# Kernel optimization log

Hardware: AMD Instinct MI355X
Metric: run time of the kernel (lower is better)

Reference implementation:

```python
import jax, jax.numpy as jnp
import numpy as np

PAD_IDX = 0
VOCAB = 60
HIDDEN = 128
BATCH = 1024
SEQ = 256


def setup_inputs() -> dict:
    key = jax.random.key(0)
    ks = jax.random.split(key, 6)
    x = jax.random.randint(ks[0], (BATCH, SEQ), 0, VOCAB, dtype=jnp.int64 if jax.config.jax_enable_x64 else jnp.int32)
    lengths = jax.random.randint(ks[1], (BATCH,), 1, SEQ + 1, dtype=x.dtype)
    emb = jax.random.normal(ks[2], (VOCAB, HIDDEN), dtype=jnp.float32) * 0.1
    emb = emb.at[PAD_IDX].set(0.0)  # nn.Embedding padding_idx row is zero
    W_ih = jax.random.normal(ks[3], (HIDDEN, HIDDEN), dtype=jnp.float32) * (1.0 / np.sqrt(HIDDEN))
    W_hh = jax.random.normal(ks[4], (HIDDEN, HIDDEN), dtype=jnp.float32) * (1.0 / np.sqrt(HIDDEN))
    W_fc = jax.random.normal(ks[5], (VOCAB, HIDDEN), dtype=jnp.float32) * (1.0 / np.sqrt(HIDDEN))
    b_fc = jnp.zeros((VOCAB,), dtype=jnp.float32)
    return {"x": x, "lengths": lengths, "emb": emb, "W_ih": W_ih,
            "W_hh": W_hh, "W_fc": W_fc, "b_fc": b_fc}


def reference(x, lengths, emb, W_ih, W_hh, W_fc, b_fc):
    embedded = emb[x]                      # [B, T, H]
    B = embedded.shape[0]
    h0 = jnp.zeros((B, HIDDEN), dtype=embedded.dtype)

    def step(h_prev, x_t):
        # z_t = x_t @ W_ih^T + h_prev @ W_hh^T ; h_t = tanh(z_t)
        h_t = jnp.tanh(x_t @ W_ih.T + h_prev @ W_hh.T)
        return h_t, h_t

    _, hs = jax.lax.scan(step, h0, jnp.swapaxes(embedded, 0, 1))  # hs: [T, B, H]
    outputs = jnp.swapaxes(hs, 0, 1)       # [B, T, H]
    last_out = jnp.take_along_axis(outputs, (lengths - 1)[:, None, None], axis=1)[:, 0, :]  # [B, H]
    return last_out @ W_fc.T + b_fc[None, :]
```

## Files before the change

### kernel.cpp

```cpp
#include <hip/hip_runtime.h>
#include <hip/hip_bf16.h>

#define BATCH 1024
#define SEQ 256
#define HIDDEN 128
#define VOCAB 60
#define MTILE 16
#define ASTRIDE 136
#define XSTRIDE (SEQ + 1)

typedef _Float16 f16x8 __attribute__((ext_vector_type(8)));
typedef _Float16 f16x4 __attribute__((ext_vector_type(4)));
typedef float f32x4 __attribute__((ext_vector_type(4)));

__device__ __forceinline__ float fast_tanh(float x) {
    float e = __builtin_amdgcn_exp2f(x * 2.8853900817779268f);
    return __builtin_fmaf(-2.0f, __builtin_amdgcn_rcpf(e + 1.0f), 1.0f);
}

__global__ void rnn_prep_embw(const float* __restrict__ emb,
                              const float* __restrict__ W_ih,
                              float* __restrict__ embW) {
    const int v = blockIdx.x;
    const int i = threadIdx.x;
    __shared__ __align__(16) float e[HIDDEN];
    e[i] = emb[v * HIDDEN + i];
    __syncthreads();
    const float4* wrow = (const float4*)(W_ih + i * HIDDEN);
    const float4* e4 = (const float4*)e;
    float a0 = 0.f, a1 = 0.f, a2 = 0.f, a3 = 0.f;
#pragma unroll
    for (int j = 0; j < HIDDEN / 4; ++j) {
        float4 w = wrow[j];
        float4 h = e4[j];
        a0 += w.x * h.x; a1 += w.y * h.y; a2 += w.z * h.z; a3 += w.w * h.w;
    }
    embW[v * HIDDEN + i] = (a0 + a1) + (a2 + a3);
}

__global__ void __launch_bounds__(256)
rnn_mfma(const int* __restrict__ x, const int* __restrict__ lengths,
         const float* __restrict__ embW, const float* __restrict__ W_hh,
         const float* __restrict__ W_fc, const float* __restrict__ b_fc,
         float* __restrict__ out) {
    const int tid = threadIdx.x;
    const int wave = tid >> 6;
    const int lane = tid & 63;
    const int q = lane >> 4;
    const int r16 = lane & 15;
    const int c0 = wave * 32;
    const int b0 = blockIdx.x * MTILE;

    __shared__ __align__(16) _Float16 Ah[2][MTILE][ASTRIDE];
    __shared__ int xs[MTILE][XSTRIDE];
    __shared__ __align__(16) float hfin[MTILE][HIDDEN];
    __shared__ int lenbuf[MTILE];

    for (int idx = tid; idx < MTILE * SEQ; idx += 256) {
        int r = idx >> 8, t = idx & (SEQ - 1);
        xs[r][t] = x[(b0 + r) * SEQ + t];
    }
    if (tid < MTILE) lenbuf[tid] = lengths[b0 + tid];

    for (int idx = tid; idx < 2 * MTILE * ASTRIDE; idx += 256)
        ((_Float16*)Ah)[idx] = (_Float16)0.0f;

    f16x8 Wf[2][4];
#pragma unroll
    for (int nt = 0; nt < 2; ++nt) {
        const float* wrow = W_hh + (c0 + 16 * nt + r16) * HIDDEN + q * 8;
#pragma unroll
        for (int kc = 0; kc < 4; ++kc) {
            const float* p = wrow + kc * 32;
#pragma unroll
            for (int j = 0; j < 8; ++j) Wf[nt][kc][j] = (_Float16)p[j];
        }
    }

    __syncthreads();

    const int mylen = lenbuf[r16];
    int lenmax = 0;
    for (int r = 0; r < MTILE; ++r) lenmax = max(lenmax, lenbuf[r]);

    {
    }
    int tok0 = xs[r16][0];
    const float* eb0 = embW + tok0 * HIDDEN + c0 + 4 * q;
    f32x4 pre0 = *(const f32x4*)eb0;
    f32x4 pre1 = *(const f32x4*)(eb0 + 16);
    int tokn = xs[r16][1 < lenmax ? 1 : 0];

    int cur = 0;
    f32x4 hout0 = {0.f, 0.f, 0.f, 0.f}, hout1 = {0.f, 0.f, 0.f, 0.f};

    for (int t = 0; t < lenmax; ++t) {
        const _Float16* arow = &Ah[cur][r16][q * 8];
        f16x8 H0 = *(const f16x8*)(arow + 0);
        f16x8 H1 = *(const f16x8*)(arow + 32);
        f16x8 H2 = *(const f16x8*)(arow + 64);
        f16x8 H3 = *(const f16x8*)(arow + 96);

        const float* eb = embW + tokn * HIDDEN + c0 + 4 * q;
        f32x4 pn0 = *(const f32x4*)eb;
        f32x4 pn1 = *(const f32x4*)(eb + 16);
        const int t2 = (t + 2 < lenmax) ? t + 2 : lenmax - 1;
        tokn = xs[r16][t2];

        f32x4 a0 = pre0, a1 = pre1;
        f32x4 d0 = {0.f, 0.f, 0.f, 0.f}, d1 = {0.f, 0.f, 0.f, 0.f};
        a0 = __builtin_amdgcn_mfma_f32_16x16x32_f16(Wf[0][0], H0, a0, 0, 0, 0);
        a1 = __builtin_amdgcn_mfma_f32_16x16x32_f16(Wf[1][0], H0, a1, 0, 0, 0);
        d0 = __builtin_amdgcn_mfma_f32_16x16x32_f16(Wf[0][2], H2, d0, 0, 0, 0);
        d1 = __builtin_amdgcn_mfma_f32_16x16x32_f16(Wf[1][2], H2, d1, 0, 0, 0);
        a0 = __builtin_amdgcn_mfma_f32_16x16x32_f16(Wf[0][1], H1, a0, 0, 0, 0);
        a1 = __builtin_amdgcn_mfma_f32_16x16x32_f16(Wf[1][1], H1, a1, 0, 0, 0);
        d0 = __builtin_amdgcn_mfma_f32_16x16x32_f16(Wf[0][3], H3, d0, 0, 0, 0);
        d1 = __builtin_amdgcn_mfma_f32_16x16x32_f16(Wf[1][3], H3, d1, 0, 0, 0);
        f32x4 z0 = a0 + d0;
        f32x4 z1 = a1 + d1;

        f32x4 th0, th1;
#pragma unroll
        for (int v = 0; v < 4; ++v) {
            th0[v] = fast_tanh(z0[v]);
            th1[v] = fast_tanh(z1[v]);
        }
        if (t + 1 == mylen) { hout0 = th0; hout1 = th1; }

        const int nxt = cur ^ 1;
        f16x4 w0, w1;
#pragma unroll
        for (int v = 0; v < 4; ++v) {
            w0[v] = (_Float16)th0[v];
            w1[v] = (_Float16)th1[v];
        }
        *(f16x4*)&Ah[nxt][r16][c0 + 4 * q] = w0;
        *(f16x4*)&Ah[nxt][r16][c0 + 16 + 4 * q] = w1;
        __syncthreads();
        cur = nxt;
        pre0 = pn0; pre1 = pn1;
    }

#pragma unroll
    for (int v = 0; v < 4; ++v) {
        hfin[r16][c0 + 4 * q + v] = hout0[v];
        hfin[r16][c0 + 16 + 4 * q + v] = hout1[v];
    }
    __syncthreads();

    const int r = tid >> 4;
    const int vbase = tid & 15;
    const float4* hv = (const float4*)hfin[r];
    for (int vo = vbase; vo < VOCAB; vo += 16) {
        const float4* wf = (const float4*)(W_fc + vo * HIDDEN);
        float a0 = 0.f, a1 = 0.f, a2 = 0.f, a3 = 0.f;
#pragma unroll
        for (int j = 0; j < HIDDEN / 4; ++j) {
            float4 a = hv[j];
            float4 w = wf[j];
            a0 += a.x * w.x; a1 += a.y * w.y; a2 += a.z * w.z; a3 += a.w * w.w;
        }
        out[(b0 + r) * VOCAB + vo] = (a0 + a1) + (a2 + a3) + b_fc[vo];
    }
}

extern "C" void kernel_launch(void* const* d_in, const int* in_sizes, int n_in,
                              void* d_out, int out_size, void* d_ws, size_t ws_size,
                              hipStream_t stream) {
    const int* x = (const int*)d_in[0];
    const int* lengths = (const int*)d_in[1];
    const float* emb = (const float*)d_in[2];
    const float* W_ih = (const float*)d_in[3];
    const float* W_hh = (const float*)d_in[4];
    const float* W_fc = (const float*)d_in[5];
    const float* b_fc = (const float*)d_in[6];
    float* out = (float*)d_out;

    float* embW = (float*)d_ws;

    rnn_prep_embw<<<VOCAB, HIDDEN, 0, stream>>>(emb, W_ih, embW);
    rnn_mfma<<<BATCH / MTILE, 256, 0, stream>>>(x, lengths, embW, W_hh, W_fc, b_fc, out);
}
```

Baseline: 193.5 us.

## Pack four 16-row batch tiles per 1024-thread block, read tokens from global

Each block now handles 64 batch rows with 16 waves (four 16-row groups sharing the same W_hh column split), so the grid shrinks from 64 to 16 blocks. Token indices are read directly from global memory instead of being staged into shared memory. The tanh outputs are packed to f16 with cvt_pkrtz, and the final hidden state is kept in f16 for the FC layer. Only 16 blocks on a many-CU GPU leaves most CUs idle. Each block's loop also runs to the longest sequence among 64 rows, and one block-wide barrier now syncs 16 waves per step, so this risks a slower recurrence.

```diff
diff --git a/kernel.cpp b/kernel.cpp
--- a/kernel.cpp
+++ b/kernel.cpp
@@ -5,12 +5,13 @@
 #define SEQ 256
 #define HIDDEN 128
 #define VOCAB 60
-#define MTILE 16
+#define NT 4
+#define MROWS (NT * 16)
 #define ASTRIDE 136
-#define XSTRIDE (SEQ + 1)
 
 typedef _Float16 f16x8 __attribute__((ext_vector_type(8)));
 typedef _Float16 f16x4 __attribute__((ext_vector_type(4)));
+typedef _Float16 f16x2 __attribute__((ext_vector_type(2)));
 typedef float f32x4 __attribute__((ext_vector_type(4)));
 
 __device__ __forceinline__ float fast_tanh(float x) {
@@ -38,32 +39,30 @@
     embW[v * HIDDEN + i] = (a0 + a1) + (a2 + a3);
 }
 
-__global__ void __launch_bounds__(256)
+__global__ void __launch_bounds__(1024)
 rnn_mfma(const int* __restrict__ x, const int* __restrict__ lengths,
          const float* __restrict__ embW, const float* __restrict__ W_hh,
          const float* __restrict__ W_fc, const float* __restrict__ b_fc,
          float* __restrict__ out) {
     const int tid = threadIdx.x;
     const int wave = tid >> 6;
+    const int tt = wave >> 2;
+    const int wq = wave & 3;
     const int lane = tid & 63;
     const int q = lane >> 4;
     const int r16 = lane & 15;
-    const int c0 = wave * 32;
-    const int b0 = blockIdx.x * MTILE;
+    const int c0 = wq * 32;
+    const int b0 = blockIdx.x * MROWS;
+    const int rloc = tt * 16 + r16;
+    const int row = b0 + rloc;
 
-    __shared__ __align__(16) _Float16 Ah[2][MTILE][ASTRIDE];
-    __shared__ int xs[MTILE][XSTRIDE];
-    __shared__ __align__(16) float hfin[MTILE][HIDDEN];
-    __shared__ int lenbuf[MTILE];
+    __shared__ __align__(16) _Float16 Ah[2][NT][16][ASTRIDE];
+    __shared__ __align__(16) _Float16 hfin[MROWS][HIDDEN];
+    __shared__ int lenbuf[MROWS];
 
-    for (int idx = tid; idx < MTILE * SEQ; idx += 256) {
-        int r = idx >> 8, t = idx & (SEQ - 1);
-        xs[r][t] = x[(b0 + r) * SEQ + t];
-    }
-    if (tid < MTILE) lenbuf[tid] = lengths[b0 + tid];
-
-    for (int idx = tid; idx < 2 * MTILE * ASTRIDE; idx += 256)
-        ((_Float16*)Ah)[idx] = (_Float16)0.0f;
+    if (tid < MROWS) lenbuf[tid] = lengths[b0 + tid];
+    for (int idx = tid; idx < (int)(sizeof(Ah) / 4); idx += 1024)
+        ((int*)Ah)[idx] = 0;
 
     f16x8 Wf[2][4];
 #pragma unroll
@@ -79,23 +78,22 @@
 
     __syncthreads();
 
-    const int mylen = lenbuf[r16];
     int lenmax = 0;
-    for (int r = 0; r < MTILE; ++r) lenmax = max(lenmax, lenbuf[r]);
+    for (int r = 0; r < MROWS; ++r) lenmax = max(lenmax, lenbuf[r]);
+    const int mylen = lenbuf[rloc];
 
-    {
-    }
-    int tok0 = xs[r16][0];
+    const int* xrow = x + row * SEQ;
+    int tok0 = xrow[0];
     const float* eb0 = embW + tok0 * HIDDEN + c0 + 4 * q;
     f32x4 pre0 = *(const f32x4*)eb0;
     f32x4 pre1 = *(const f32x4*)(eb0 + 16);
-    int tokn = xs[r16][1 < lenmax ? 1 : 0];
+    int tokn = xrow[lenmax > 1 ? 1 : 0];
 
+    uint2 hA = {0u, 0u}, hB = {0u, 0u};
     int cur = 0;
-    f32x4 hout0 = {0.f, 0.f, 0.f, 0.f}, hout1 = {0.f, 0.f, 0.f, 0.f};
 
     for (int t = 0; t < lenmax; ++t) {
-        const _Float16* arow = &Ah[cur][r16][q * 8];
+        const _Float16* arow = &Ah[cur][tt][r16][q * 8];
         f16x8 H0 = *(const f16x8*)(arow + 0);
         f16x8 H1 = *(const f16x8*)(arow + 32);
         f16x8 H2 = *(const f16x8*)(arow + 64);
@@ -105,7 +103,7 @@
         f32x4 pn0 = *(const f32x4*)eb;
         f32x4 pn1 = *(const f32x4*)(eb + 16);
         const int t2 = (t + 2 < lenmax) ? t + 2 : lenmax - 1;
-        tokn = xs[r16][t2];
+        const int tok2 = xrow[t2];
 
         f32x4 a0 = pre0, a1 = pre1;
         f32x4 d0 = {0.f, 0.f, 0.f, 0.f}, d1 = {0.f, 0.f, 0.f, 0.f};
@@ -120,46 +118,43 @@
         f32x4 z0 = a0 + d0;
         f32x4 z1 = a1 + d1;
 
-        f32x4 th0, th1;
-#pragma unroll
-        for (int v = 0; v < 4; ++v) {
-            th0[v] = fast_tanh(z0[v]);
-            th1[v] = fast_tanh(z1[v]);
-        }
-        if (t + 1 == mylen) { hout0 = th0; hout1 = th1; }
+        float t00 = fast_tanh(z0[0]), t01 = fast_tanh(z0[1]);
+        float t02 = fast_tanh(z0[2]), t03 = fast_tanh(z0[3]);
+        float t10 = fast_tanh(z1[0]), t11 = fast_tanh(z1[1]);
+        float t12 = fast_tanh(z1[2]), t13 = fast_tanh(z1[3]);
+
+        uint2 pk0, pk1;
+        pk0.x = __builtin_bit_cast(unsigned int, __builtin_amdgcn_cvt_pkrtz(t00, t01));
+        pk0.y = __builtin_bit_cast(unsigned int, __builtin_amdgcn_cvt_pkrtz(t02, t03));
+        pk1.x = __builtin_bit_cast(unsigned int, __builtin_amdgcn_cvt_pkrtz(t10, t11));
+        pk1.y = __builtin_bit_cast(unsigned int, __builtin_amdgcn_cvt_pkrtz(t12, t13));
+
+        if (t + 1 == mylen) { hA = pk0; hB = pk1; }
 
         const int nxt = cur ^ 1;
-        f16x4 w0, w1;
-#pragma unroll
-        for (int v = 0; v < 4; ++v) {
-            w0[v] = (_Float16)th0[v];
-            w1[v] = (_Float16)th1[v];
-        }
-        *(f16x4*)&Ah[nxt][r16][c0 + 4 * q] = w0;
-        *(f16x4*)&Ah[nxt][r16][c0 + 16 + 4 * q] = w1;
+        *(uint2*)&Ah[nxt][tt][r16][c0 + 4 * q] = pk0;
+        *(uint2*)&Ah[nxt][tt][r16][c0 + 16 + 4 * q] = pk1;
         __syncthreads();
         cur = nxt;
-        pre0 = pn0; pre1 = pn1;
+        pre0 = pn0; pre1 = pn1; tokn = tok2;
     }
 
-#pragma unroll
-    for (int v = 0; v < 4; ++v) {
-        hfin[r16][c0 + 4 * q + v] = hout0[v];
-        hfin[r16][c0 + 16 + 4 * q + v] = hout1[v];
-    }
+    *(uint2*)&hfin[rloc][c0 + 4 * q] = hA;
+    *(uint2*)&hfin[rloc][c0 + 16 + 4 * q] = hB;
     __syncthreads();
 
     const int r = tid >> 4;
-    const int vbase = tid & 15;
-    const float4* hv = (const float4*)hfin[r];
-    for (int vo = vbase; vo < VOCAB; vo += 16) {
+    const int vb = tid & 15;
+    const _Float16* hr = hfin[r];
+    for (int vo = vb; vo < VOCAB; vo += 16) {
         const float4* wf = (const float4*)(W_fc + vo * HIDDEN);
         float a0 = 0.f, a1 = 0.f, a2 = 0.f, a3 = 0.f;
 #pragma unroll
         for (int j = 0; j < HIDDEN / 4; ++j) {
-            float4 a = hv[j];
             float4 w = wf[j];
-            a0 += a.x * w.x; a1 += a.y * w.y; a2 += a.z * w.z; a3 += a.w * w.w;
+            f16x4 hh = *(const f16x4*)(hr + 4 * j);
+            a0 += w.x * (float)hh[0]; a1 += w.y * (float)hh[1];
+            a2 += w.z * (float)hh[2]; a3 += w.w * (float)hh[3];
         }
         out[(b0 + r) * VOCAB + vo] = (a0 + a1) + (a2 + a3) + b_fc[vo];
     }
@@ -180,5 +175,5 @@
     float* embW = (float*)d_ws;
 
     rnn_prep_embw<<<VOCAB, HIDDEN, 0, stream>>>(emb, W_ih, embW);
-    rnn_mfma<<<BATCH / MTILE, 256, 0, stream>>>(x, lengths, embW, W_hh, W_fc, b_fc, out);
+    rnn_mfma<<<BATCH / MROWS, 1024, 0, stream>>>(x, lengths, embW, W_hh, W_fc, b_fc, out);
 }
```

Result: slower. 523.9 us (+170.7%).
